# Kernel tuning notes

Hardware: AMD Instinct MI355X
Metric: run time of the kernel (lower is better)

Reference implementation:

```python
import jax, jax.numpy as jnp
import numpy as np

B, N, D, H = 1, 4096, 512, 8
HD = D // H


def setup_inputs() -> dict:
    key = jax.random.key(0)
    ks = jax.random.split(key, 12)
    s = 0.02  # weight init scale for numerical stability
    query = jax.random.normal(ks[0], (B, N, D), jnp.float32)
    key_t = jax.random.normal(ks[1], (B, N, D), jnp.float32)
    value = jax.random.normal(ks[2], (B, N, D), jnp.float32)
    Wq = jax.random.normal(ks[3], (D, D), jnp.float32) * s
    bq = jax.random.normal(ks[4], (D,), jnp.float32) * s
    Wk = jax.random.normal(ks[5], (D, D), jnp.float32) * s
    bk = jax.random.normal(ks[6], (D,), jnp.float32) * s
    Wv = jax.random.normal(ks[7], (D, D), jnp.float32) * s
    bv = jax.random.normal(ks[8], (D,), jnp.float32) * s
    Wo = jax.random.normal(ks[9], (D, D), jnp.float32) * s
    bo = jax.random.normal(ks[10], (D,), jnp.float32) * s
    # build sgconv_mat exactly as __init__: shifted nonneg adjacency, max-normalized,
    # then symmetric degree normalization D^-1/2 A D^-1/2 (gwmha_layer_num=1)
    A = jax.random.uniform(ks[11], (N, N), jnp.float32)
    A = A + A.min()
    A = A / A.max()
    deg = A.sum(1)
    dinv = 1.0 / jnp.sqrt(deg)
    sgconv_mat = (dinv[:, None] * A * dinv[None, :])[None]  # [1,N,N]
    return {"query": query, "key": key_t, "value": value,
            "Wq": Wq, "bq": bq, "Wk": Wk, "bk": bk, "Wv": Wv, "bv": bv,
            "Wo": Wo, "bo": bo, "sgconv_mat": sgconv_mat}


def reference(query, key, value, Wq, bq, Wk, bk, Wv, bv, Wo, bo, sgconv_mat):
    b, n, d = query.shape
    q = (query @ Wq.T + bq).reshape(b, n, H, HD)
    k = (key @ Wk.T + bk).reshape(b, n, H, HD)
    v = (value @ Wv.T + bv).reshape(b, n, H, HD)
    energy = jnp.einsum('bqhd,bkhd->bhqk', q, k)
    attn = jax.nn.softmax(energy / jnp.sqrt(jnp.float32(d)), axis=3)
    out = jnp.einsum('bhqk,bkhd->bqhd', attn, v).reshape(b, n, d)
    out = sgconv_mat @ out          # [1,N,N] @ [B,N,D] -> [B,N,D]
    return out @ Wo.T + bo
```

## Files before the change

### kernel.cpp

```cpp
#include <hip/hip_runtime.h>
#include <hip/hip_bf16.h>
#include <math.h>

typedef __bf16 bf16_t;
typedef __bf16 bf16x8 __attribute__((ext_vector_type(8)));
typedef unsigned short ushort8v __attribute__((ext_vector_type(8)));
typedef float floatx4 __attribute__((ext_vector_type(4)));

static __device__ inline unsigned short f2bf_rne(float f) {
    unsigned int u = __builtin_bit_cast(unsigned int, f);
    unsigned int r = u + 0x7FFFu + ((u >> 16) & 1u);
    return (unsigned short)(r >> 16);
}
static __device__ inline bf16_t f2bf(float f) {
    return __builtin_bit_cast(bf16_t, f2bf_rne(f));
}

static __device__ inline void store_c(float* C, size_t i, float v) { C[i] = v; }
static __device__ inline void store_c(bf16_t* C, size_t i, float v) { C[i] = f2bf(v); }

static __device__ inline void cvt8(const float* src, bf16_t* dst, size_t idx) {
    float4 a = *(const float4*)(src + idx);
    float4 c = *(const float4*)(src + idx + 4);
    ushort8v u;
    u[0] = f2bf_rne(a.x); u[1] = f2bf_rne(a.y); u[2] = f2bf_rne(a.z); u[3] = f2bf_rne(a.w);
    u[4] = f2bf_rne(c.x); u[5] = f2bf_rne(c.y); u[6] = f2bf_rne(c.z); u[7] = f2bf_rne(c.w);
    *(ushort8v*)(dst + idx) = u;
}

template <typename TC>
__device__ inline void gemm_body(
    const bf16_t* __restrict__ A, int lda,
    const bf16_t* __restrict__ B, int ldb,
    const float* __restrict__ bias_col, const float* __restrict__ bias_row,
    TC* __restrict__ C, int ldc, int K, int m0, int n0)
{
    __shared__ bf16_t As[128 * 68];
    __shared__ bf16_t Bs[64 * 68];

    const int tid = threadIdx.x;
    const int lane = tid & 63, wave = tid >> 6;
    const int wm = wave & 1, wn = wave >> 1;
    const int lo16 = lane & 15, quad = lane >> 4;
    const int sr = tid >> 2, sc = (tid & 3) * 8;

    floatx4 acc[4][2] = {};

    for (int k0 = 0; k0 < K; k0 += 32) {
        bf16x8 a0 = *(const bf16x8*)(A + (size_t)(m0 + sr) * lda + k0 + sc);
        bf16x8 a1 = *(const bf16x8*)(A + (size_t)(m0 + 64 + sr) * lda + k0 + sc);
        bf16x8 b0 = *(const bf16x8*)(B + (size_t)(n0 + sr) * ldb + k0 + sc);
        __syncthreads();
        *(bf16x8*)(&As[sr * 68 + sc]) = a0;
        *(bf16x8*)(&As[(64 + sr) * 68 + sc]) = a1;
        *(bf16x8*)(&Bs[sr * 68 + sc]) = b0;
        __syncthreads();

        bf16x8 af[4], bfv[2];
#pragma unroll
        for (int mt = 0; mt < 4; ++mt)
            af[mt] = *(const bf16x8*)(&As[(wm * 64 + mt * 16 + lo16) * 68 + quad * 8]);
#pragma unroll
        for (int nt = 0; nt < 2; ++nt)
            bfv[nt] = *(const bf16x8*)(&Bs[(wn * 32 + nt * 16 + lo16) * 68 + quad * 8]);
#pragma unroll
        for (int mt = 0; mt < 4; ++mt)
#pragma unroll
            for (int nt = 0; nt < 2; ++nt)
                acc[mt][nt] = __builtin_amdgcn_mfma_f32_16x16x32_bf16(
                    af[mt], bfv[nt], acc[mt][nt], 0, 0, 0);
    }

#pragma unroll
    for (int nt = 0; nt < 2; ++nt) {
        const int gn = n0 + wn * 32 + nt * 16 + lo16;
        const float bc = bias_col ? bias_col[gn] : 0.f;
#pragma unroll
        for (int mt = 0; mt < 4; ++mt) {
#pragma unroll
            for (int r = 0; r < 4; ++r) {
                const int gm = m0 + wm * 64 + mt * 16 + quad * 4 + r;
                float v = acc[mt][nt][r] + bc;
                if (bias_row) v += bias_row[gm];
                store_c(C, (size_t)gm * ldc + gn, v);
            }
        }
    }
}

__global__ __launch_bounds__(256) void prep(
    const float* __restrict__ query, const float* __restrict__ key, const float* __restrict__ value,
    const float* __restrict__ Wq, const float* __restrict__ Wk,
    const float* __restrict__ Wv, const float* __restrict__ Wo,
    bf16_t* qB, bf16_t* kB, bf16_t* vB,
    bf16_t* wqB, bf16_t* wkB, bf16_t* wvB, bf16_t* woB)
{
    const int b = blockIdx.x;
    const float* src; bf16_t* dst; size_t base;
    if      (b < 256) { src = query; dst = qB;  base = (size_t)b * 8192; }
    else if (b < 512) { src = key;   dst = kB;  base = (size_t)(b - 256) * 8192; }
    else if (b < 768) { src = value; dst = vB;  base = (size_t)(b - 512) * 8192; }
    else if (b < 800) { src = Wq;    dst = wqB; base = (size_t)(b - 768) * 8192; }
    else if (b < 832) { src = Wk;    dst = wkB; base = (size_t)(b - 800) * 8192; }
    else if (b < 864) { src = Wv;    dst = wvB; base = (size_t)(b - 832) * 8192; }
    else              { src = Wo;    dst = woB; base = (size_t)(b - 864) * 8192; }
#pragma unroll
    for (int it = 0; it < 4; ++it)
        cvt8(src, dst, base + (size_t)it * 2048 + threadIdx.x * 8);
}

__global__ __launch_bounds__(256) void proj_qkv(
    const bf16_t* __restrict__ qB, const bf16_t* __restrict__ wqB, const float* __restrict__ bq,
    const bf16_t* __restrict__ kB, const bf16_t* __restrict__ wkB, const float* __restrict__ bk,
    const bf16_t* __restrict__ wvB, const bf16_t* __restrict__ vB, const float* __restrict__ bv,
    const float* __restrict__ sg, bf16_t* __restrict__ sgb,
    bf16_t* __restrict__ q, bf16_t* __restrict__ k, bf16_t* __restrict__ vt)
{
    const int b = blockIdx.x;
    if (b >= 768) {
        const size_t base = (size_t)(b - 768) * 8192;
#pragma unroll
        for (int it = 0; it < 4; ++it)
            cvt8(sg, sgb, base + (size_t)it * 2048 + threadIdx.x * 8);
        return;
    }
    const bf16_t *A, *B;
    const float *bc = nullptr, *br = nullptr;
    bf16_t* C;
    int ldc = 512, m0, n0;
    if (b < 512) {
        int i = b & 255, x = i & 7, t = i >> 3;
        n0 = (t & 7) * 64;
        m0 = ((t >> 3) * 8 + x) * 128;
        if (b < 256) { A = qB; B = wqB; bc = bq; C = q; }
        else         { A = kB; B = wkB; bc = bk; C = k; }
    } else {
        int i = b - 512;
        n0 = (i & 63) * 64;
        m0 = (i >> 6) * 128;
        A = wvB; B = vB; br = bv; C = vt; ldc = 4096;
    }
    gemm_body<bf16_t>(A, 512, B, 512, bc, br, C, ldc, 512, m0, n0);
}

__global__ __launch_bounds__(256) void sgconv_gemm(
    const bf16_t* __restrict__ sgb, const bf16_t* __restrict__ aot,
    float* __restrict__ part)
{
    const int i = blockIdx.x & 127;
    const int kb = blockIdx.x >> 7;
    const int ms = i & 31, ns = i >> 5;
    const int m0 = ms * 128, n0 = ns * 128;
    const int kbase = kb * 1024;

    __shared__ bf16_t As[128 * 68];
    __shared__ bf16_t Bs[128 * 68];

    const int tid = threadIdx.x;
    const int lane = tid & 63, wave = tid >> 6;
    const int wm = wave & 1, wn = wave >> 1;
    const int lo16 = lane & 15, quad = lane >> 4;
    const int sr = tid >> 1, sc = (tid & 1) * 16;

    const bf16_t* asrc = sgb + (size_t)(m0 + sr) * 4096 + kbase + sc;
    const bf16_t* bsrc = aot + (size_t)(n0 + sr) * 4096 + kbase + sc;

    floatx4 acc[4][4] = {};

    for (int k0 = 0; k0 < 1024; k0 += 32) {
        bf16x8 a0 = *(const bf16x8*)(asrc + k0);
        bf16x8 a1 = *(const bf16x8*)(asrc + k0 + 8);
        bf16x8 b0 = *(const bf16x8*)(bsrc + k0);
        bf16x8 b1 = *(const bf16x8*)(bsrc + k0 + 8);
        __syncthreads();
        *(bf16x8*)(&As[sr * 68 + sc]) = a0;
        *(bf16x8*)(&As[sr * 68 + sc + 8]) = a1;
        *(bf16x8*)(&Bs[sr * 68 + sc]) = b0;
        *(bf16x8*)(&Bs[sr * 68 + sc + 8]) = b1;
        __syncthreads();

        bf16x8 af[4], bfv[4];
#pragma unroll
        for (int mt = 0; mt < 4; ++mt)
            af[mt] = *(const bf16x8*)(&As[(wm * 64 + mt * 16 + lo16) * 68 + quad * 8]);
#pragma unroll
        for (int nt = 0; nt < 4; ++nt)
            bfv[nt] = *(const bf16x8*)(&Bs[(wn * 64 + nt * 16 + lo16) * 68 + quad * 8]);
#pragma unroll
        for (int mt = 0; mt < 4; ++mt)
#pragma unroll
            for (int nt = 0; nt < 4; ++nt)
                acc[mt][nt] = __builtin_amdgcn_mfma_f32_16x16x32_bf16(
                    af[mt], bfv[nt], acc[mt][nt], 0, 0, 0);
    }

    float* pw = part + (size_t)kb * (4096 * 512);
#pragma unroll
    for (int mt = 0; mt < 4; ++mt)
#pragma unroll
        for (int r = 0; r < 4; ++r) {
            const int gm = m0 + wm * 64 + mt * 16 + quad * 4 + r;
#pragma unroll
            for (int nt = 0; nt < 4; ++nt)
                pw[(size_t)gm * 512 + n0 + wn * 64 + nt * 16 + lo16] = acc[mt][nt][r];
        }
}

__global__ __launch_bounds__(256) void part_reduce(
    const float* __restrict__ p, bf16_t* __restrict__ o2)
{
    const size_t S = (size_t)4096 * 512;
    const size_t idx = ((size_t)blockIdx.x * 256 + threadIdx.x) * 8;
    ushort8v u;
#pragma unroll
    for (int half = 0; half < 2; ++half) {
        float4 s = *(const float4*)(p + idx + half * 4);
#pragma unroll
        for (int kb = 1; kb < 4; ++kb) {
            float4 t = *(const float4*)(p + kb * S + idx + half * 4);
            s.x += t.x; s.y += t.y; s.z += t.z; s.w += t.w;
        }
        u[half * 4 + 0] = f2bf_rne(s.x);
        u[half * 4 + 1] = f2bf_rne(s.y);
        u[half * 4 + 2] = f2bf_rne(s.z);
        u[half * 4 + 3] = f2bf_rne(s.w);
    }
    *(ushort8v*)(o2 + idx) = u;
}

__global__ __launch_bounds__(256) void out_proj(
    const bf16_t* __restrict__ o2, const bf16_t* __restrict__ woB,
    const float* __restrict__ bo, float* __restrict__ out)
{
    const int i = blockIdx.x, x = i & 7, t = i >> 3;
    const int n0 = (t & 7) * 64, m0 = ((t >> 3) * 8 + x) * 128;
    gemm_body<float>(o2, 512, woB, 512, bo, nullptr, out, 512, 512, m0, n0);
}

__global__ __launch_bounds__(256, 4) void flash_attn(
    const bf16_t* __restrict__ q, const bf16_t* __restrict__ kk,
    const bf16_t* __restrict__ vt, float* __restrict__ op,
    float* __restrict__ lp, float scale)
{
    const int N = 4096, D = 512;
    const int h   = blockIdx.x & 7;
    const int qb  = (blockIdx.x >> 3) & 31;
    const int qtr = blockIdx.x >> 8;
    const int t0  = qtr * 1024;

    const int tid = threadIdx.x;
    const int w = tid >> 6, lane = tid & 63;
    const int lo16 = lane & 15, quad = lane >> 4;

    __shared__ bf16_t Ks[64 * 72];
    __shared__ bf16_t Vs[64 * 72];
    __shared__ bf16_t Ps[4][32 * 72];

    const bf16_t* qp = q + (size_t)(qb * 128 + w * 32 + lo16) * D + h * 64 + quad * 8;
    bf16x8 qf[2][2];
    qf[0][0] = *(const bf16x8*)qp;
    qf[0][1] = *(const bf16x8*)(qp + 32);
    qf[1][0] = *(const bf16x8*)(qp + 16 * D);
    qf[1][1] = *(const bf16x8*)(qp + 16 * D + 32);

    const int srow = tid >> 2, sc = (tid & 3) * 16;
    const bf16_t* ksrc = kk + (size_t)(t0 + srow) * D + h * 64 + sc;
    const bf16_t* vsrc = vt + (size_t)(h * 64 + srow) * N + t0 + sc;
    bf16_t* kdst = &Ks[srow * 72 + sc];
    bf16_t* vdst = &Vs[srow * 72 + sc];

    floatx4 o[4][2] = {};
    float l[2] = {0.f, 0.f};

    bf16x8 kr0 = *(const bf16x8*)ksrc;
    bf16x8 kr1 = *(const bf16x8*)(ksrc + 8);
    bf16x8 vr0 = *(const bf16x8*)vsrc;
    bf16x8 vr1 = *(const bf16x8*)(vsrc + 8);

    for (int it = 0; it < 16; ++it) {
        __syncthreads();
        *(bf16x8*)kdst = kr0;  *(bf16x8*)(kdst + 8) = kr1;
        *(bf16x8*)vdst = vr0;  *(bf16x8*)(vdst + 8) = vr1;
        __syncthreads();
        if (it < 15) {
            const bf16_t* kn = ksrc + (size_t)(it + 1) * 64 * D;
            const bf16_t* vn = vsrc + (it + 1) * 64;
            kr0 = *(const bf16x8*)kn;  kr1 = *(const bf16x8*)(kn + 8);
            vr0 = *(const bf16x8*)vn;  vr1 = *(const bf16x8*)(vn + 8);
        }

        floatx4 s[4][2];
#pragma unroll
        for (int tt = 0; tt < 4; ++tt) {
            bf16x8 kf0 = *(const bf16x8*)(&Ks[(tt * 16 + lo16) * 72 + quad * 8]);
            bf16x8 kf1 = *(const bf16x8*)(&Ks[(tt * 16 + lo16) * 72 + 32 + quad * 8]);
#pragma unroll
            for (int qt = 0; qt < 2; ++qt) {
                floatx4 a = {};
                a = __builtin_amdgcn_mfma_f32_16x16x32_bf16(kf0, qf[qt][0], a, 0, 0, 0);
                a = __builtin_amdgcn_mfma_f32_16x16x32_bf16(kf1, qf[qt][1], a, 0, 0, 0);
                s[tt][qt] = a;
            }
        }
#pragma unroll
        for (int tt = 0; tt < 4; ++tt)
#pragma unroll
            for (int qt = 0; qt < 2; ++qt) {
                float e0 = __expf(s[tt][qt][0] * scale);
                float e1 = __expf(s[tt][qt][1] * scale);
                float e2 = __expf(s[tt][qt][2] * scale);
                float e3 = __expf(s[tt][qt][3] * scale);
                l[qt] += (e0 + e1) + (e2 + e3);
                uint2 pk;
                pk.x = (unsigned)f2bf_rne(e0) | ((unsigned)f2bf_rne(e1) << 16);
                pk.y = (unsigned)f2bf_rne(e2) | ((unsigned)f2bf_rne(e3) << 16);
                *(uint2*)(&Ps[w][(qt * 16 + lo16) * 72 + tt * 16 + quad * 4]) = pk;
            }
#pragma unroll
        for (int ks = 0; ks < 2; ++ks) {
            bf16x8 pf0 = *(const bf16x8*)(&Ps[w][lo16 * 72 + ks * 32 + quad * 8]);
            bf16x8 pf1 = *(const bf16x8*)(&Ps[w][(16 + lo16) * 72 + ks * 32 + quad * 8]);
#pragma unroll
            for (int t = 0; t < 4; ++t) {
                bf16x8 vf = *(const bf16x8*)(&Vs[(t * 16 + lo16) * 72 + ks * 32 + quad * 8]);
                o[t][0] = __builtin_amdgcn_mfma_f32_16x16x32_bf16(vf, pf0, o[t][0], 0, 0, 0);
                o[t][1] = __builtin_amdgcn_mfma_f32_16x16x32_bf16(vf, pf1, o[t][1], 0, 0, 0);
            }
        }
    }

#pragma unroll
    for (int qt = 0; qt < 2; ++qt) {
        l[qt] += __shfl_xor(l[qt], 16);
        l[qt] += __shfl_xor(l[qt], 32);
    }

    const int g = blockIdx.x & 255;
    float* opw = op + ((size_t)qtr * 256 + g) * 8192;
#pragma unroll
    for (int t = 0; t < 4; ++t)
#pragma unroll
        for (int pt = 0; pt < 2; ++pt)
#pragma unroll
            for (int r = 0; r < 4; ++r)
                opw[(t * 16 + quad * 4 + r) * 128 + w * 32 + pt * 16 + lo16] = o[t][pt][r];

    if (quad == 0) {
        float* lpw = lp + ((size_t)qtr * 256 + g) * 128;
        lpw[w * 32 + lo16] = l[0];
        lpw[w * 32 + 16 + lo16] = l[1];
    }
}

__global__ __launch_bounds__(256) void attn_combine(
    const float* __restrict__ op, const float* __restrict__ lp, bf16_t* __restrict__ aot)
{
    const int g = blockIdx.x;
    const int h = g & 7, qb = g >> 3;
    const int tid = threadIdx.x;
    __shared__ float ls[128];
    if (tid < 128) {
        float s = 0.f;
#pragma unroll
        for (int qtr = 0; qtr < 4; ++qtr)
            s += lp[((size_t)qtr * 256 + g) * 128 + tid];
        ls[tid] = 1.0f / s;
    }
    __syncthreads();
    const float* b0 = op + (size_t)g * 8192;
    const size_t QS = (size_t)256 * 8192;
#pragma unroll 4
    for (int i = 0; i < 32; ++i) {
        int idx = i * 256 + tid;
        float v = b0[idx] + b0[QS + idx] + b0[2 * QS + idx] + b0[3 * QS + idx];
        int dim = idx >> 7, qc = idx & 127;
        aot[(size_t)(h * 64 + dim) * 4096 + qb * 128 + qc] = f2bf(v * ls[qc]);
    }
}

extern "C" void kernel_launch(void* const* d_in, const int* in_sizes, int n_in,
                              void* d_out, int out_size, void* d_ws, size_t ws_size,
                              hipStream_t stream)
{
    const int N = 4096, D = 512;
    const float* query = (const float*)d_in[0];
    const float* key_t = (const float*)d_in[1];
    const float* value = (const float*)d_in[2];
    const float* Wq = (const float*)d_in[3];
    const float* bq = (const float*)d_in[4];
    const float* Wk = (const float*)d_in[5];
    const float* bk = (const float*)d_in[6];
    const float* Wv = (const float*)d_in[7];
    const float* bv = (const float*)d_in[8];
    const float* Wo = (const float*)d_in[9];
    const float* bo = (const float*)d_in[10];
    const float* sg = (const float*)d_in[11];
    float* out = (float*)d_out;

    const size_t ND = (size_t)N * D;
    const size_t DD = (size_t)D * D;

    char* base = (char*)d_ws;
    bf16_t* q    = (bf16_t*)base;
    bf16_t* kk   = q   + ND;
    bf16_t* vt   = kk  + ND;
    bf16_t* aot  = vt  + ND;
    bf16_t* sgb  = aot + ND;
    char* regA   = (char*)(sgb + (size_t)N * N);
    bf16_t* qB   = (bf16_t*)regA;
    bf16_t* kB   = qB + ND;
    bf16_t* vB   = kB + ND;
    bf16_t* wqB  = vB + ND;
    bf16_t* wkB  = wqB + DD;
    bf16_t* wvB  = wkB + DD;
    float* op    = (float*)regA;
    float* p     = (float*)regA;
    char* tail   = regA + (size_t)4 * 256 * 8192 * 4;
    float*  lp   = (float*)tail;
    bf16_t* woB  = (bf16_t*)(lp + (size_t)4 * 256 * 128);
    bf16_t* o2   = woB + DD;

    const dim3 blk(256);

    prep<<<896, blk, 0, stream>>>(query, key_t, value, Wq, Wk, Wv, Wo,
                                  qB, kB, vB, wqB, wkB, wvB, woB);

    proj_qkv<<<2816, blk, 0, stream>>>(qB, wqB, bq, kB, wkB, bk,
                                       wvB, vB, bv, sg, sgb, q, kk, vt);

    const float scale = 1.0f / sqrtf((float)D);
    flash_attn<<<1024, blk, 0, stream>>>(q, kk, vt, op, lp, scale);
    attn_combine<<<256, blk, 0, stream>>>(op, lp, aot);

    sgconv_gemm<<<512, blk, 0, stream>>>(sgb, aot, p);
    part_reduce<<<1024, blk, 0, stream>>>(p, o2);
    out_proj<<<256, blk, 0, stream>>>(o2, woB, bo, out);

    (void)in_sizes; (void)n_in; (void)out_size; (void)ws_size;
}
```

Baseline: 262.9 us.

## Rebalance kernel grids: move sgconv conversion into attention, smaller GEMM tiles

```diff
diff --git a/kernel.cpp b/kernel.cpp
--- a/kernel.cpp
+++ b/kernel.cpp
@@ -113,17 +113,9 @@
     const bf16_t* __restrict__ qB, const bf16_t* __restrict__ wqB, const float* __restrict__ bq,
     const bf16_t* __restrict__ kB, const bf16_t* __restrict__ wkB, const float* __restrict__ bk,
     const bf16_t* __restrict__ wvB, const bf16_t* __restrict__ vB, const float* __restrict__ bv,
-    const float* __restrict__ sg, bf16_t* __restrict__ sgb,
     bf16_t* __restrict__ q, bf16_t* __restrict__ k, bf16_t* __restrict__ vt)
 {
     const int b = blockIdx.x;
-    if (b >= 768) {
-        const size_t base = (size_t)(b - 768) * 8192;
-#pragma unroll
-        for (int it = 0; it < 4; ++it)
-            cvt8(sg, sgb, base + (size_t)it * 2048 + threadIdx.x * 8);
-        return;
-    }
     const bf16_t *A, *B;
     const float *bc = nullptr, *br = nullptr;
     bf16_t* C;
@@ -147,63 +139,13 @@
     const bf16_t* __restrict__ sgb, const bf16_t* __restrict__ aot,
     float* __restrict__ part)
 {
-    const int i = blockIdx.x & 127;
-    const int kb = blockIdx.x >> 7;
+    const int i = blockIdx.x & 255;
+    const int kb = blockIdx.x >> 8;
     const int ms = i & 31, ns = i >> 5;
-    const int m0 = ms * 128, n0 = ns * 128;
+    const int m0 = ms * 128, n0 = ns * 64;
     const int kbase = kb * 1024;
-
-    __shared__ bf16_t As[128 * 68];
-    __shared__ bf16_t Bs[128 * 68];
-
-    const int tid = threadIdx.x;
-    const int lane = tid & 63, wave = tid >> 6;
-    const int wm = wave & 1, wn = wave >> 1;
-    const int lo16 = lane & 15, quad = lane >> 4;
-    const int sr = tid >> 1, sc = (tid & 1) * 16;
-
-    const bf16_t* asrc = sgb + (size_t)(m0 + sr) * 4096 + kbase + sc;
-    const bf16_t* bsrc = aot + (size_t)(n0 + sr) * 4096 + kbase + sc;
-
-    floatx4 acc[4][4] = {};
-
-    for (int k0 = 0; k0 < 1024; k0 += 32) {
-        bf16x8 a0 = *(const bf16x8*)(asrc + k0);
-        bf16x8 a1 = *(const bf16x8*)(asrc + k0 + 8);
-        bf16x8 b0 = *(const bf16x8*)(bsrc + k0);
-        bf16x8 b1 = *(const bf16x8*)(bsrc + k0 + 8);
-        __syncthreads();
-        *(bf16x8*)(&As[sr * 68 + sc]) = a0;
-        *(bf16x8*)(&As[sr * 68 + sc + 8]) = a1;
-        *(bf16x8*)(&Bs[sr * 68 + sc]) = b0;
-        *(bf16x8*)(&Bs[sr * 68 + sc + 8]) = b1;
-        __syncthreads();
-
-        bf16x8 af[4], bfv[4];
-#pragma unroll
-        for (int mt = 0; mt < 4; ++mt)
-            af[mt] = *(const bf16x8*)(&As[(wm * 64 + mt * 16 + lo16) * 68 + quad * 8]);
-#pragma unroll
-        for (int nt = 0; nt < 4; ++nt)
-            bfv[nt] = *(const bf16x8*)(&Bs[(wn * 64 + nt * 16 + lo16) * 68 + quad * 8]);
-#pragma unroll
-        for (int mt = 0; mt < 4; ++mt)
-#pragma unroll
-            for (int nt = 0; nt < 4; ++nt)
-                acc[mt][nt] = __builtin_amdgcn_mfma_f32_16x16x32_bf16(
-                    af[mt], bfv[nt], acc[mt][nt], 0, 0, 0);
-    }
-
-    float* pw = part + (size_t)kb * (4096 * 512);
-#pragma unroll
-    for (int mt = 0; mt < 4; ++mt)
-#pragma unroll
-        for (int r = 0; r < 4; ++r) {
-            const int gm = m0 + wm * 64 + mt * 16 + quad * 4 + r;
-#pragma unroll
-            for (int nt = 0; nt < 4; ++nt)
-                pw[(size_t)gm * 512 + n0 + wn * 64 + nt * 16 + lo16] = acc[mt][nt][r];
-        }
+    gemm_body<float>(sgb + kbase, 4096, aot + kbase, 4096, nullptr, nullptr,
+                     part + (size_t)kb * (4096 * 512), 512, 1024, m0, n0);
 }
 
 __global__ __launch_bounds__(256) void part_reduce(
@@ -233,15 +175,71 @@
     const float* __restrict__ bo, float* __restrict__ out)
 {
     const int i = blockIdx.x, x = i & 7, t = i >> 3;
-    const int n0 = (t & 7) * 64, m0 = ((t >> 3) * 8 + x) * 128;
-    gemm_body<float>(o2, 512, woB, 512, bo, nullptr, out, 512, 512, m0, n0);
+    const int n0 = (t & 7) * 64;
+    const int m0 = ((t >> 3) * 8 + x) * 64;
+
+    __shared__ bf16_t As[64 * 68];
+    __shared__ bf16_t Bs[64 * 68];
+
+    const int tid = threadIdx.x;
+    const int lane = tid & 63, wave = tid >> 6;
+    const int wm = wave & 1, wn = wave >> 1;
+    const int lo16 = lane & 15, quad = lane >> 4;
+    const int sr = tid >> 2, sc = (tid & 3) * 8;
+
+    floatx4 acc[2][2] = {};
+
+    for (int k0 = 0; k0 < 512; k0 += 32) {
+        bf16x8 a0 = *(const bf16x8*)(o2 + (size_t)(m0 + sr) * 512 + k0 + sc);
+        bf16x8 b0 = *(const bf16x8*)(woB + (size_t)(n0 + sr) * 512 + k0 + sc);
+        __syncthreads();
+        *(bf16x8*)(&As[sr * 68 + sc]) = a0;
+        *(bf16x8*)(&Bs[sr * 68 + sc]) = b0;
+        __syncthreads();
+
+        bf16x8 af[2], bfv[2];
+#pragma unroll
+        for (int mt = 0; mt < 2; ++mt)
+            af[mt] = *(const bf16x8*)(&As[(wm * 32 + mt * 16 + lo16) * 68 + quad * 8]);
+#pragma unroll
+        for (int nt = 0; nt < 2; ++nt)
+            bfv[nt] = *(const bf16x8*)(&Bs[(wn * 32 + nt * 16 + lo16) * 68 + quad * 8]);
+#pragma unroll
+        for (int mt = 0; mt < 2; ++mt)
+#pragma unroll
+            for (int nt = 0; nt < 2; ++nt)
+                acc[mt][nt] = __builtin_amdgcn_mfma_f32_16x16x32_bf16(
+                    af[mt], bfv[nt], acc[mt][nt], 0, 0, 0);
+    }
+
+#pragma unroll
+    for (int nt = 0; nt < 2; ++nt) {
+        const int gn = n0 + wn * 32 + nt * 16 + lo16;
+        const float bc = bo[gn];
+#pragma unroll
+        for (int mt = 0; mt < 2; ++mt)
+#pragma unroll
+            for (int r = 0; r < 4; ++r) {
+                const int gm = m0 + wm * 32 + mt * 16 + quad * 4 + r;
+                out[(size_t)gm * 512 + gn] = acc[mt][nt][r] + bc;
+            }
+    }
 }
 
 __global__ __launch_bounds__(256, 4) void flash_attn(
     const bf16_t* __restrict__ q, const bf16_t* __restrict__ kk,
     const bf16_t* __restrict__ vt, float* __restrict__ op,
-    float* __restrict__ lp, float scale)
-{
+    float* __restrict__ lp, float scale,
+    const float* __restrict__ sg, bf16_t* __restrict__ sgb)
+{
+    if (blockIdx.x >= 1024) {
+        const size_t base = (size_t)(blockIdx.x - 1024) * 8192;
+#pragma unroll
+        for (int it = 0; it < 4; ++it)
+            cvt8(sg, sgb, base + (size_t)it * 2048 + threadIdx.x * 8);
+        return;
+    }
+
     const int N = 4096, D = 512;
     const int h   = blockIdx.x & 7;
     const int qb  = (blockIdx.x >> 3) & 31;
@@ -425,16 +423,16 @@
     prep<<<896, blk, 0, stream>>>(query, key_t, value, Wq, Wk, Wv, Wo,
                                   qB, kB, vB, wqB, wkB, wvB, woB);
 
-    proj_qkv<<<2816, blk, 0, stream>>>(qB, wqB, bq, kB, wkB, bk,
-                                       wvB, vB, bv, sg, sgb, q, kk, vt);
+    proj_qkv<<<768, blk, 0, stream>>>(qB, wqB, bq, kB, wkB, bk,
+                                      wvB, vB, bv, q, kk, vt);
 
     const float scale = 1.0f / sqrtf((float)D);
-    flash_attn<<<1024, blk, 0, stream>>>(q, kk, vt, op, lp, scale);
+    flash_attn<<<3072, blk, 0, stream>>>(q, kk, vt, op, lp, scale, sg, sgb);
     attn_combine<<<256, blk, 0, stream>>>(op, lp, aot);
 
-    sgconv_gemm<<<512, blk, 0, stream>>>(sgb, aot, p);
+    sgconv_gemm<<<1024, blk, 0, stream>>>(sgb, aot, p);
     part_reduce<<<1024, blk, 0, stream>>>(p, o2);
-    out_proj<<<256, blk, 0, stream>>>(o2, woB, bo, out);
+    out_proj<<<512, blk, 0, stream>>>(o2, woB, bo, out);
 
     (void)in_sizes; (void)n_in; (void)out_size; (void)ws_size;
 }
```

After: 252.7 us. 1.04x faster.
